# Kernel tuning notes

Measured on AMD Instinct MI355X. Metric: run time of the kernel, lower is better.

Reference implementation:

```python
import jax, jax.numpy as jnp
import numpy as np

NI, ND, NH = 64, 64, 4
NB, NLOC, NNEI = 4, 2048, 64


def setup_inputs() -> dict:
    key = jax.random.key(0)
    ks = jax.random.split(key, 7)
    g1 = jax.random.normal(ks[0], (NB, NLOC, NI), dtype=jnp.float32)
    gg1 = jax.random.normal(ks[1], (NB, NLOC, NNEI, NI), dtype=jnp.float32)
    nlist_mask = jax.random.randint(ks[2], (NB, NLOC, NNEI), 0, 2).astype(bool)
    # torch Linear weight (out, in); store transposed for x @ W
    Wq = jax.random.normal(ks[3], (NI, ND * NH), dtype=jnp.float32) * (1.0 / np.sqrt(NI))
    Wkv = jax.random.normal(ks[4], (NI, (ND + NI) * NH), dtype=jnp.float32) * (1.0 / np.sqrt(NI))
    Wh = jax.random.normal(ks[5], (NI * NH, NI), dtype=jnp.float32) * (1.0 / np.sqrt(NI * NH))
    bh = jax.random.normal(ks[6], (NI,), dtype=jnp.float32) * 0.01
    return {"g1": g1, "gg1": gg1, "nlist_mask": nlist_mask,
            "Wq": Wq, "Wkv": Wkv, "Wh": Wh, "bh": bh}


def reference(g1, gg1, nlist_mask, Wq, Wkv, Wh, bh):
    nb, nloc, nnei = nlist_mask.shape
    ni, nd, nh = NI, ND, NH
    # q: (nb, nloc, nh, nd)
    q = (g1 @ Wq).reshape(nb, nloc, nd, nh).transpose(0, 1, 3, 2)
    # kv: (nb, nloc, nnei, nd, 2*nh) -> (nb, nloc, 2*nh, nnei, nd); valid since ni == nd
    kv = (gg1 @ Wkv).reshape(nb, nloc, nnei, nd, 2 * nh).transpose(0, 1, 4, 2, 3)
    k = kv[:, :, :nh]          # (nb, nloc, nh, nnei, nd)
    v = kv[:, :, nh:2 * nh]    # (nb, nloc, nh, nnei, nd)
    attnw = jnp.einsum('blhd,blhjd->blhj', q, k) / np.sqrt(nd).astype(np.float32)
    m = nlist_mask[:, :, None, :]  # (nb, nloc, 1, nnei)
    attnw = jnp.where(m, attnw, -jnp.inf)
    attnw = jax.nn.softmax(attnw, axis=-1)
    attnw = jnp.where(m, attnw, 0.0)
    ret = jnp.einsum('blhj,blhjd->blhd', attnw, v).reshape(nb, nloc, nh * ni)
    return ret @ Wh + bh
```

## Files before the change

### kernel.cpp

```cpp
#include <hip/hip_runtime.h>
#include <hip/hip_fp16.h>
#include <math.h>

#define NATOM 8192

namespace {

typedef _Float16 half8 __attribute__((ext_vector_type(8)));
typedef _Float16 half2t __attribute__((ext_vector_type(2)));
typedef float f32x4 __attribute__((ext_vector_type(4)));

#define LDS_FENCE()                                        \
  do {                                                     \
    asm volatile("s_waitcnt lgkmcnt(0)" ::: "memory");     \
    __builtin_amdgcn_sched_barrier(0);                     \
  } while (0)

__global__ void pack_weights(const float* __restrict__ Wq,
                             const float* __restrict__ Wkv,
                             const float* __restrict__ Wh,
                             _Float16* __restrict__ out) {
  int tid = blockIdx.x * 256 + threadIdx.x;
  if (tid < 16384) {
    int r = tid >> 6, ip = tid & 63;
    int h = r >> 6, i = r & 63;
    float acc = 0.f;
#pragma unroll 8
    for (int d = 0; d < 64; ++d)
      acc += Wq[ip * 256 + d * 4 + h] * Wkv[i * 512 + d * 8 + h];
    int mt = r >> 4, m = r & 15;
    int ks = ip >> 5, kk = ip & 31, lqk = kk >> 3, e = kk & 7;
    int l = lqk * 16 + m;
    out[(((mt * 2 + ks) * 64) + l) * 8 + e] = (_Float16)acc;
  } else {
    int idx = tid - 16384;
    int c = idx >> 8, k2 = idx & 255;
    int h = k2 >> 6, i = k2 & 63;
    float acc = 0.f;
#pragma unroll 8
    for (int d = 0; d < 64; ++d)
      acc += Wkv[i * 512 + d * 8 + 4 + h] * Wh[(h * 64 + d) * 64 + c];
    int mt2 = c >> 4, m = c & 15;
    int ks2 = k2 >> 5, kk = k2 & 31, lqk = kk >> 3, e = kk & 7;
    int l = lqk * 16 + m;
    out[16384 + (((mt2 * 8 + ks2) * 64) + l) * 8 + e] = (_Float16)acc;
  }
}

__device__ __forceinline__ half8 cvt8(float4 a, float4 b) {
  half8 r;
  r[0] = (_Float16)a.x; r[1] = (_Float16)a.y; r[2] = (_Float16)a.z; r[3] = (_Float16)a.w;
  r[4] = (_Float16)b.x; r[5] = (_Float16)b.y; r[6] = (_Float16)b.z; r[7] = (_Float16)b.w;
  return r;
}

__global__ __launch_bounds__(256, 4)
void local_atten_kernel(const float* __restrict__ g1,
                        const float* __restrict__ gg1,
                        const int* __restrict__ mask,
                        const _Float16* __restrict__ wpack,
                        const float* __restrict__ bh,
                        float* __restrict__ out) {
  __shared__ __align__(16) _Float16 qa[4][1536];

  const _Float16* Mp = wpack;
  const _Float16* Wp = wpack + 16384;

  const int t = threadIdx.x;
  const int lane = t & 63;
  const int wave = t >> 6;
  const int lq = lane >> 4;
  const int lr = lane & 15;
  const int atom = blockIdx.x * 4 + wave;

  _Float16* qaw = qa[wave];
  const float* gbase = gg1 + (size_t)atom * 4096;

  int mreg[4];
#pragma unroll
  for (int jt = 0; jt < 4; ++jt)
    mreg[jt] = mask[(size_t)atom * 64 + jt * 16 + lr];

  float bhv[4];
#pragma unroll
  for (int mt2 = 0; mt2 < 4; ++mt2) bhv[mt2] = bh[mt2 * 16 + lr];

  qaw[1152 + lane] = (_Float16)g1[(size_t)atom * 64 + lane];

#pragma unroll
  for (int r = 4; r < 16; ++r) qaw[r * 72 + lane] = (_Float16)0.f;

  float4 cur[4];
  {
    const float4* p = reinterpret_cast<const float4*>(gbase + lr * 64 + lq * 8);
    cur[0] = p[0]; cur[1] = p[1]; cur[2] = p[8]; cur[3] = p[9];
  }

  LDS_FENCE();

  {
    const half8* mp = reinterpret_cast<const half8*>(Mp);
    half8 ag0 = *reinterpret_cast<const half8*>(qaw + 1152 + lq * 8);
    half8 ag1 = *reinterpret_cast<const half8*>(qaw + 1152 + 32 + lq * 8);
#pragma unroll 4
    for (int mt = 0; mt < 16; ++mt) {
      f32x4 acc = {0.f, 0.f, 0.f, 0.f};
      acc = __builtin_amdgcn_mfma_f32_16x16x32_f16(ag0, mp[(mt * 2) * 64 + lane], acc, 0, 0, 0);
      acc = __builtin_amdgcn_mfma_f32_16x16x32_f16(ag1, mp[(mt * 2 + 1) * 64 + lane], acc, 0, 0, 0);
      if (lq == 0)
        qaw[(mt >> 2) * 72 + (mt & 3) * 16 + lr] = (_Float16)acc[0];
    }
  }

  LDS_FENCE();

  half8 A0 = *reinterpret_cast<const half8*>(qaw + lr * 72 + lq * 8);
  half8 A1 = *reinterpret_cast<const half8*>(qaw + lr * 72 + 32 + lq * 8);

  f32x4 sa[4];
#pragma unroll
  for (int jt = 0; jt < 4; ++jt) {
    float4 nxt[4];
    if (jt < 3) {
      const float4* p =
          reinterpret_cast<const float4*>(gbase + ((jt + 1) * 16 + lr) * 64 + lq * 8);
      nxt[0] = p[0]; nxt[1] = p[1]; nxt[2] = p[8]; nxt[3] = p[9];
    }
    half8 b0 = cvt8(cur[0], cur[1]);
    half8 b1 = cvt8(cur[2], cur[3]);
    f32x4 acc = {0.f, 0.f, 0.f, 0.f};
    acc = __builtin_amdgcn_mfma_f32_16x16x32_f16(A0, b0, acc, 0, 0, 0);
    acc = __builtin_amdgcn_mfma_f32_16x16x32_f16(A1, b1, acc, 0, 0, 0);
    sa[jt] = acc;
    if (jt < 3) { cur[0] = nxt[0]; cur[1] = nxt[1]; cur[2] = nxt[2]; cur[3] = nxt[3]; }
  }

  float fT[16];
#pragma unroll
  for (int ks = 0; ks < 2; ++ks) {
    const float* gks = gbase + (ks * 32 + lq * 8) * 64 + lr;
#pragma unroll
    for (int e = 0; e < 8; ++e) fT[ks * 8 + e] = gks[e * 64];
  }

  float awv[4][4];
#pragma unroll
  for (int r = 0; r < 4; ++r) {
    float x[4];
#pragma unroll
    for (int jt = 0; jt < 4; ++jt)
      x[jt] = mreg[jt] ? sa[jt][r] * 0.125f : -INFINITY;
    float mx = fmaxf(fmaxf(x[0], x[1]), fmaxf(x[2], x[3]));
#pragma unroll
    for (int off = 8; off > 0; off >>= 1) mx = fmaxf(mx, __shfl_xor(mx, off));
    float p[4], sum = 0.f;
#pragma unroll
    for (int jt = 0; jt < 4; ++jt) {
      p[jt] = mreg[jt] ? __expf(x[jt] - mx) : 0.f;
      sum += p[jt];
    }
#pragma unroll
    for (int off = 8; off > 0; off >>= 1) sum += __shfl_xor(sum, off);
    float inv = (sum > 0.f) ? (1.f / sum) : 0.f;
#pragma unroll
    for (int jt = 0; jt < 4; ++jt) awv[r][jt] = p[jt] * inv;
  }
  if (lq == 0) {
#pragma unroll
    for (int r = 0; r < 4; ++r)
#pragma unroll
      for (int jt = 0; jt < 4; ++jt)
        qaw[r * 72 + jt * 16 + lr] = (_Float16)awv[r][jt];
  }

  LDS_FENCE();

  half8 Au0 = *reinterpret_cast<const half8*>(qaw + lr * 72 + lq * 8);
  half8 Au1 = *reinterpret_cast<const half8*>(qaw + lr * 72 + 32 + lq * 8);

  f32x4 ua[4];
#pragma unroll
  for (int it = 0; it < 4; ++it) {
    float fN[16];
    if (it < 3) {
#pragma unroll
      for (int ks = 0; ks < 2; ++ks) {
        const float* gks = gbase + (ks * 32 + lq * 8) * 64 + (it + 1) * 16 + lr;
#pragma unroll
        for (int e = 0; e < 8; ++e) fN[ks * 8 + e] = gks[e * 64];
      }
    }
    half8 b0, b1;
#pragma unroll
    for (int e = 0; e < 8; ++e) { b0[e] = (_Float16)fT[e]; b1[e] = (_Float16)fT[8 + e]; }
    f32x4 acc = {0.f, 0.f, 0.f, 0.f};
    acc = __builtin_amdgcn_mfma_f32_16x16x32_f16(Au0, b0, acc, 0, 0, 0);
    acc = __builtin_amdgcn_mfma_f32_16x16x32_f16(Au1, b1, acc, 0, 0, 0);
    ua[it] = acc;
    if (it < 3) {
#pragma unroll
      for (int e = 0; e < 16; ++e) fT[e] = fN[e];
    }
  }

  if (lq == 0) {
#pragma unroll
    for (int r = 0; r < 4; ++r)
#pragma unroll
      for (int it = 0; it < 4; ++it)
        qaw[1216 + r * 64 + it * 16 + lr] = (_Float16)ua[it][r];
  }

  LDS_FENCE();

  {
    const half8* wp = reinterpret_cast<const half8*>(Wp);
    half8 au[8];
#pragma unroll
    for (int ks2 = 0; ks2 < 8; ++ks2)
      au[ks2] = *reinterpret_cast<const half8*>(qaw + 1216 + ks2 * 32 + lq * 8);
#pragma unroll 1
    for (int mt2 = 0; mt2 < 4; ++mt2) {
      f32x4 aa = {0.f, 0.f, 0.f, 0.f}, ab = {0.f, 0.f, 0.f, 0.f};
#pragma unroll
      for (int ks2 = 0; ks2 < 4; ++ks2) {
        aa = __builtin_amdgcn_mfma_f32_16x16x32_f16(au[ks2], wp[(mt2 * 8 + ks2) * 64 + lane], aa, 0, 0, 0);
        ab = __builtin_amdgcn_mfma_f32_16x16x32_f16(au[4 + ks2], wp[(mt2 * 8 + 4 + ks2) * 64 + lane], ab, 0, 0, 0);
      }
      if (lq == 0)
        out[(size_t)atom * 64 + mt2 * 16 + lr] = aa[0] + ab[0] + bhv[mt2];
    }
  }
}

}

extern "C" void kernel_launch(void* const* d_in, const int* in_sizes, int n_in,
                              void* d_out, int out_size, void* d_ws, size_t ws_size,
                              hipStream_t stream) {
  const float* g1   = (const float*)d_in[0];
  const float* gg1  = (const float*)d_in[1];
  const int*   mask = (const int*)d_in[2];
  const float* Wq   = (const float*)d_in[3];
  const float* Wkv  = (const float*)d_in[4];
  const float* Wh   = (const float*)d_in[5];
  const float* bh   = (const float*)d_in[6];
  float* out = (float*)d_out;
  (void)in_sizes; (void)n_in; (void)ws_size; (void)out_size;

  _Float16* wpack = (_Float16*)d_ws;
  pack_weights<<<128, 256, 0, stream>>>(Wq, Wkv, Wh, wpack);
  local_atten_kernel<<<NATOM / 4, 256, 0, stream>>>(g1, gg1, mask, wpack, bh, out);
}
```

Measured before the change: 234.3 us.

## Issue all gg1 tile loads up front instead of one-ahead prefetch

All four 16-neighbour tiles of gg1 for the score stage are now loaded at kernel start, before the q projection, rather than double-buffered one tile ahead. All four transposed tiles for the value stage are also loaded before the softmax. This gives more memory-level parallelism and hides load latency behind the projection and softmax work. The cost is much higher register pressure (64+64 floats live), which under launch_bounds(256,4) may cause spills or lower occupancy.

```diff
diff --git a/kernel.cpp b/kernel.cpp
--- a/kernel.cpp
+++ b/kernel.cpp
@@ -87,14 +87,16 @@
 
   qaw[1152 + lane] = (_Float16)g1[(size_t)atom * 64 + lane];
 
+  float4 cur[4][4];
+#pragma unroll
+  for (int jt = 0; jt < 4; ++jt) {
+    const float4* p =
+        reinterpret_cast<const float4*>(gbase + (jt * 16 + lr) * 64 + lq * 8);
+    cur[jt][0] = p[0]; cur[jt][1] = p[1]; cur[jt][2] = p[8]; cur[jt][3] = p[9];
+  }
+
 #pragma unroll
   for (int r = 4; r < 16; ++r) qaw[r * 72 + lane] = (_Float16)0.f;
-
-  float4 cur[4];
-  {
-    const float4* p = reinterpret_cast<const float4*>(gbase + lr * 64 + lq * 8);
-    cur[0] = p[0]; cur[1] = p[1]; cur[2] = p[8]; cur[3] = p[9];
-  }
 
   LDS_FENCE();
 
@@ -120,27 +122,23 @@
   f32x4 sa[4];
 #pragma unroll
   for (int jt = 0; jt < 4; ++jt) {
-    float4 nxt[4];
-    if (jt < 3) {
-      const float4* p =
-          reinterpret_cast<const float4*>(gbase + ((jt + 1) * 16 + lr) * 64 + lq * 8);
-      nxt[0] = p[0]; nxt[1] = p[1]; nxt[2] = p[8]; nxt[3] = p[9];
-    }
-    half8 b0 = cvt8(cur[0], cur[1]);
-    half8 b1 = cvt8(cur[2], cur[3]);
+    half8 b0 = cvt8(cur[jt][0], cur[jt][1]);
+    half8 b1 = cvt8(cur[jt][2], cur[jt][3]);
     f32x4 acc = {0.f, 0.f, 0.f, 0.f};
     acc = __builtin_amdgcn_mfma_f32_16x16x32_f16(A0, b0, acc, 0, 0, 0);
     acc = __builtin_amdgcn_mfma_f32_16x16x32_f16(A1, b1, acc, 0, 0, 0);
     sa[jt] = acc;
-    if (jt < 3) { cur[0] = nxt[0]; cur[1] = nxt[1]; cur[2] = nxt[2]; cur[3] = nxt[3]; }
-  }
-
-  float fT[16];
-#pragma unroll
-  for (int ks = 0; ks < 2; ++ks) {
-    const float* gks = gbase + (ks * 32 + lq * 8) * 64 + lr;
-#pragma unroll
-    for (int e = 0; e < 8; ++e) fT[ks * 8 + e] = gks[e * 64];
+  }
+
+  float fU[4][16];
+#pragma unroll
+  for (int it = 0; it < 4; ++it) {
+#pragma unroll
+    for (int ks = 0; ks < 2; ++ks) {
+      const float* gks = gbase + (ks * 32 + lq * 8) * 64 + it * 16 + lr;
+#pragma unroll
+      for (int e = 0; e < 8; ++e) fU[it][ks * 8 + e] = gks[e * 64];
+    }
   }
 
   float awv[4][4];
@@ -181,26 +179,16 @@
   f32x4 ua[4];
 #pragma unroll
   for (int it = 0; it < 4; ++it) {
-    float fN[16];
-    if (it < 3) {
-#pragma unroll
-      for (int ks = 0; ks < 2; ++ks) {
-        const float* gks = gbase + (ks * 32 + lq * 8) * 64 + (it + 1) * 16 + lr;
-#pragma unroll
-        for (int e = 0; e < 8; ++e) fN[ks * 8 + e] = gks[e * 64];
-      }
-    }
     half8 b0, b1;
 #pragma unroll
-    for (int e = 0; e < 8; ++e) { b0[e] = (_Float16)fT[e]; b1[e] = (_Float16)fT[8 + e]; }
+    for (int e = 0; e < 8; ++e) {
+      b0[e] = (_Float16)fU[it][e];
+      b1[e] = (_Float16)fU[it][8 + e];
+    }
     f32x4 acc = {0.f, 0.f, 0.f, 0.f};
     acc = __builtin_amdgcn_mfma_f32_16x16x32_f16(Au0, b0, acc, 0, 0, 0);
     acc = __builtin_amdgcn_mfma_f32_16x16x32_f16(Au1, b1, acc, 0, 0, 0);
     ua[it] = acc;
-    if (it < 3) {
-#pragma unroll
-      for (int e = 0; e < 16; ++e) fT[e] = fN[e];
-    }
   }
 
   if (lq == 0) {
```

New measurement: 233.9 us. About the same (-0.2%).
